# Kernel optimization log

Measured on AMD Instinct MI355X. Metric: run time of the kernel, lower is better.

## Reference

```python
import jax, jax.numpy as jnp
import numpy as np

WS = 8          # window side -> N = 64
DIM = 512
NH = 16
B_ = 1024       # batch * num_windows
CPB_HIDDEN = 512


def _make_coords_table():
    # relative_coords_table: (1, 2*WS-1, 2*WS-1, 2), log-spaced continuous coords
    r = np.arange(-(WS - 1), WS, dtype=np.float32)
    t = np.stack(np.meshgrid(r, r, indexing='ij'), axis=-1)[None]  # (1,15,15,2)
    t = t / (WS - 1)
    t = t * 8.0
    t = np.sign(t) * np.log2(np.abs(t) + 1.0) / np.log2(8.0)
    return t.astype(np.float32)


def _make_rel_pos_index():
    coords = np.stack(np.meshgrid(np.arange(WS), np.arange(WS), indexing='ij'))  # (2,WS,WS)
    cf = coords.reshape(2, -1)                       # (2, N)
    rel = (cf[:, :, None] - cf[:, None, :]).transpose(1, 2, 0).astype(np.int64)  # (N,N,2)
    rel[..., 0] += WS - 1
    rel[..., 1] += WS - 1
    rel[..., 0] *= 2 * WS - 1
    return rel.sum(-1)  # (N, N) int


def setup_inputs() -> dict:
    key = jax.random.key(0)
    ks = jax.random.split(key, 10)
    s_in = 1.0 / np.sqrt(DIM)
    inp = {
        'x': jax.random.normal(ks[0], (B_, WS * WS, DIM), dtype=jnp.float32),
        'qkv_weight': jax.random.normal(ks[1], (3 * DIM, DIM), dtype=jnp.float32) * s_in,
        'q_bias': jnp.zeros((DIM,), dtype=jnp.float32),
        'v_bias': jnp.zeros((DIM,), dtype=jnp.float32),
        'logit_scale': jnp.full((NH, 1, 1), np.log(10.0), dtype=jnp.float32),
        'cpb_w1': jax.random.normal(ks[2], (CPB_HIDDEN, 2), dtype=jnp.float32) * (1.0 / np.sqrt(2.0)),
        'cpb_b1': jnp.zeros((CPB_HIDDEN,), dtype=jnp.float32),
        'cpb_w2': jax.random.normal(ks[3], (NH, CPB_HIDDEN), dtype=jnp.float32) * (1.0 / np.sqrt(CPB_HIDDEN)),
        'proj_w': jax.random.normal(ks[4], (DIM, DIM), dtype=jnp.float32) * s_in,
        'proj_b': jnp.zeros((DIM,), dtype=jnp.float32),
        'rel_coords_table': jnp.asarray(_make_coords_table()),
        'rel_pos_index': jnp.asarray(_make_rel_pos_index()),
    }
    return inp


def reference(x, qkv_weight, q_bias, v_bias, logit_scale, cpb_w1, cpb_b1, cpb_w2,
              proj_w, proj_b, rel_coords_table, rel_pos_index):
    B, N, C = x.shape
    nh = logit_scale.shape[0]
    hd = C // nh

    # qkv projection; bias = [q_bias, 0, v_bias] (k has no bias, Swin-V2 style)
    qkv_bias = jnp.concatenate([q_bias, jnp.zeros_like(q_bias), v_bias])
    qkv = x @ qkv_weight.T + qkv_bias                       # (B, N, 3C)
    qkv = qkv.reshape(B, N, 3, nh, hd).transpose(2, 0, 3, 1, 4)  # (3, B, nh, N, hd)
    q, k, v = qkv[0], qkv[1], qkv[2]

    # continuous position bias MLP: Linear(2,512)+ReLU -> Linear(512,nh, no bias)
    hidden = jax.nn.relu(rel_coords_table @ cpb_w1.T + cpb_b1)  # (1,15,15,512)
    table = (hidden @ cpb_w2.T).reshape(-1, nh)                 # ((2W-1)^2, nh)
    rpb = table[rel_pos_index.reshape(-1)].reshape(N, N, nh).transpose(2, 0, 1)
    rpb = 16.0 * jax.nn.sigmoid(rpb)                            # (nh, N, N)

    # fused attention math: (QK^T)*logit_scale + bias -> softmax -> AV
    scores = jnp.einsum('bhnd,bhmd->bhnm', q, k) * logit_scale.reshape(1, nh, 1, 1)
    scores = scores + rpb[None]
    attn = jax.nn.softmax(scores, axis=-1)
    out = jnp.einsum('bhnm,bhmd->bhnd', attn, v)                # (B, nh, N, hd)
    out = out.transpose(0, 2, 1, 3).reshape(B, N, C)

    return out @ proj_w.T + proj_b
```

## Files before the change

### kernel.cpp

```cpp
#include <hip/hip_runtime.h>
#include <hip/hip_bf16.h>
#include <stdint.h>
#include <stddef.h>


typedef unsigned short ushort_t;
typedef _Float16 half_t;
typedef __attribute__((ext_vector_type(8))) _Float16 half8;
typedef __attribute__((ext_vector_type(4))) float f32x4;

#define MROWS 65536

__device__ __forceinline__ ushort_t h_bits(half_t h) {
  union { half_t h; ushort_t u; } c; c.h = h; return c.u;
}

__device__ __forceinline__ void gload16(const void* g, void* l) {
  __builtin_amdgcn_global_load_lds(
      (const __attribute__((address_space(1))) unsigned int*)g,
      (__attribute__((address_space(3))) unsigned int*)l, 16, 0, 0);
}

__global__ __launch_bounds__(256) void k_split(const float* __restrict__ src,
                                               ushort_t* __restrict__ hi,
                                               ushort_t* __restrict__ lo, int n4) {
  int stride = gridDim.x * blockDim.x;
  for (int i = blockIdx.x * blockDim.x + threadIdx.x; i < n4; i += stride) {
    f32x4 x = reinterpret_cast<const f32x4*>(src)[i];
    ushort_t h4[4], l4[4];
#pragma unroll
    for (int j = 0; j < 4; ++j) {
      half_t hh = (half_t)x[j];
      h4[j] = h_bits(hh);
      l4[j] = h_bits((half_t)(x[j] - (float)hh));
    }
    reinterpret_cast<uint2*>(hi)[i] =
        make_uint2(h4[0] | ((unsigned)h4[1] << 16), h4[2] | ((unsigned)h4[3] << 16));
    reinterpret_cast<uint2*>(lo)[i] =
        make_uint2(l4[0] | ((unsigned)l4[1] << 16), l4[2] | ((unsigned)l4[3] << 16));
  }
}

__global__ __launch_bounds__(256) void k_cpb1(const float* __restrict__ coords,
                                              const float* __restrict__ w1,
                                              const float* __restrict__ b1,
                                              const float* __restrict__ w2,
                                              float* __restrict__ tbl) {
  __shared__ float hid[512];
  int p = blockIdx.x;
  float c0 = coords[2 * p], c1 = coords[2 * p + 1];
  int t = threadIdx.x;
  for (int j = t; j < 512; j += 256) {
    float v = c0 * w1[2 * j] + c1 * w1[2 * j + 1] + b1[j];
    hid[j] = v > 0.f ? v : 0.f;
  }
  __syncthreads();
  int wid = t >> 6, lane = t & 63;
#pragma unroll
  for (int hh = 0; hh < 4; ++hh) {
    int head = wid * 4 + hh;
    float s = 0.f;
    for (int j = lane; j < 512; j += 64) s += hid[j] * w2[head * 512 + j];
#pragma unroll
    for (int off = 32; off > 0; off >>= 1) s += __shfl_xor(s, off);
    if (lane == 0) tbl[p * 16 + head] = 16.f / (1.f + __expf(-s));
  }
}

__global__ __launch_bounds__(256) void k_cpb2(const float* __restrict__ tbl,
                                              const int* __restrict__ ridx,
                                              float* __restrict__ rpb) {
  int idx = blockIdx.x * 256 + threadIdx.x;
  int h = idx >> 12, nm = idx & 4095;
  rpb[idx] = tbl[ridx[nm] * 16 + h];
}

__device__ __forceinline__ int swz(int c, int r) {
  return c ^ (r & 3) ^ ((r >> 2) & 3);
}

__global__ __launch_bounds__(256, 2) void k_qkv(
    const ushort_t* __restrict__ Wh, const ushort_t* __restrict__ Wl,
    const float* __restrict__ X,
    const float* __restrict__ qb, const float* __restrict__ vb,
    ushort_t* __restrict__ oqh, ushort_t* __restrict__ oql,
    ushort_t* __restrict__ okh, ushort_t* __restrict__ okl,
    ushort_t* __restrict__ ovt) {
  __shared__ ushort_t lAh[2][4096];
  __shared__ ushort_t lAl[2][4096];
  __shared__ ushort_t lBh[2][4096];
  __shared__ ushort_t lBl[2][4096];

  int nwg = gridDim.x, bid = blockIdx.x;
  int idx = ((nwg & 7) == 0) ? ((bid & 7) * (nwg >> 3) + (bid >> 3)) : bid;
  int tm = idx % 12, tn = idx / 12;
  int tid = threadIdx.x;
  int wid = tid >> 6, lane = tid & 63;
  int wr = wid >> 1, wc = wid & 1;
  int lr = lane & 15, lq = lane >> 4;

  int rA = tid >> 2, qA = tid & 3;
  size_t gA = (size_t)(tm * 128 + rA) * 512 + (swz(qA, rA) << 3);
  int dA = wid * 512;

  int rB = tid >> 3, qB = tid & 7;
  const float* gB = X + (size_t)(tn * 128 + rB) * 512 + qB * 4;
  int dB = rB * 32 + (swz(qB >> 1, rB) << 3) + ((qB & 1) << 2);

  f32x4 acc[4][4];
#pragma unroll
  for (int i = 0; i < 4; ++i)
#pragma unroll
    for (int j = 0; j < 4; ++j)
#pragma unroll
      for (int r = 0; r < 4; ++r) acc[i][j][r] = 0.f;

  auto stageA = [&](int kk, int bs) {
    gload16(Wh + gA + kk, &lAh[bs][dA]);
    gload16(Wh + gA + 32768 + kk, &lAh[bs][2048 + dA]);
    gload16(Wl + gA + kk, &lAl[bs][dA]);
    gload16(Wl + gA + 32768 + kk, &lAl[bs][2048 + dA]);
  };
  auto loadB = [&](int kk, f32x4* xr) {
#pragma unroll
    for (int s = 0; s < 4; ++s) xr[s] = *(const f32x4*)(gB + s * 16384 + kk);
  };
  auto writeB = [&](const f32x4* xr, int bs) {
#pragma unroll
    for (int s = 0; s < 4; ++s) {
      ushort_t h4[4], l4[4];
#pragma unroll
      for (int e = 0; e < 4; ++e) {
        half_t hh = (half_t)xr[s][e];
        h4[e] = h_bits(hh);
        l4[e] = h_bits((half_t)(xr[s][e] - (float)hh));
      }
      *(uint2*)&lBh[bs][dB + s * 1024] =
          make_uint2(h4[0] | ((unsigned)h4[1] << 16), h4[2] | ((unsigned)h4[3] << 16));
      *(uint2*)&lBl[bs][dB + s * 1024] =
          make_uint2(l4[0] | ((unsigned)l4[1] << 16), l4[2] | ((unsigned)l4[3] << 16));
    }
  };

  f32x4 xr[4];
  stageA(0, 0);
  loadB(0, xr);
  writeB(xr, 0);
  const int c16 = swz(lq, lr) << 3;
#pragma unroll 2
  for (int t = 0; t < 16; ++t) {
    __syncthreads();
    int bs = t & 1;
    if (t < 15) {
      stageA((t + 1) * 32, bs ^ 1);
      loadB((t + 1) * 32, xr);
    }
    half8 ah[4], al[4], bh[4], bl[4];
#pragma unroll
    for (int i = 0; i < 4; ++i) {
      int ro = (wr * 64 + i * 16 + lr) * 32 + c16;
      ah[i] = *(const half8*)&lAh[bs][ro];
      al[i] = *(const half8*)&lAl[bs][ro];
    }
#pragma unroll
    for (int j = 0; j < 4; ++j) {
      int ro = (wc * 64 + j * 16 + lr) * 32 + c16;
      bh[j] = *(const half8*)&lBh[bs][ro];
      bl[j] = *(const half8*)&lBl[bs][ro];
    }
#pragma unroll
    for (int i = 0; i < 4; ++i)
#pragma unroll
      for (int j = 0; j < 4; ++j) {
        acc[i][j] = __builtin_amdgcn_mfma_f32_16x16x32_f16(ah[i], bh[j], acc[i][j], 0, 0, 0);
        acc[i][j] = __builtin_amdgcn_mfma_f32_16x16x32_f16(ah[i], bl[j], acc[i][j], 0, 0, 0);
        acc[i][j] = __builtin_amdgcn_mfma_f32_16x16x32_f16(al[i], bh[j], acc[i][j], 0, 0, 0);
      }
    if (t < 15) writeB(xr, bs ^ 1);
  }

#pragma unroll
  for (int i = 0; i < 4; ++i) {
    int ch0 = tm * 128 + wr * 64 + i * 16 + lq * 4;
#pragma unroll
    for (int j = 0; j < 4; ++j) {
      int tok = tn * 128 + wc * 64 + j * 16 + lr;
      int sec = tm >> 2;
      int h = (ch0 >> 5) & 15, d0 = ch0 & 31;
      int win = tok >> 6, n = tok & 63;
      size_t pr = (size_t)win * 16 + h;
      f32x4 b4;
      if (sec == 0)      b4 = *(const f32x4*)&qb[ch0];
      else if (sec == 2) b4 = *(const f32x4*)&vb[ch0 - 1024];
      else { b4[0] = 0.f; b4[1] = 0.f; b4[2] = 0.f; b4[3] = 0.f; }
      if (sec == 2) {
#pragma unroll
        for (int r = 0; r < 4; ++r) {
          float v = acc[i][j][r] + b4[r];
          ovt[(pr * 32 + d0 + r) * 64 + n] = h_bits((half_t)v);
        }
      } else {
        ushort_t hb[4], lb4[4];
#pragma unroll
        for (int r = 0; r < 4; ++r) {
          float v = acc[i][j][r] + b4[r];
          half_t hh = (half_t)v;
          hb[r] = h_bits(hh);
          lb4[r] = h_bits((half_t)(v - (float)hh));
        }
        uint2 hw = make_uint2(hb[0] | ((unsigned)hb[1] << 16), hb[2] | ((unsigned)hb[3] << 16));
        uint2 lw = make_uint2(lb4[0] | ((unsigned)lb4[1] << 16), lb4[2] | ((unsigned)lb4[3] << 16));
        size_t o = (pr * 64 + n) * 32 + d0;
        if (sec == 0) { *(uint2*)&oqh[o] = hw; *(uint2*)&oql[o] = lw; }
        else          { *(uint2*)&okh[o] = hw; *(uint2*)&okl[o] = lw; }
      }
    }
  }
}

__global__ __launch_bounds__(256, 2) void k_proj(
    const ushort_t* __restrict__ Wh, const ushort_t* __restrict__ Wl,
    const ushort_t* __restrict__ Bp,
    const float* __restrict__ pb, float* __restrict__ outp) {
  __shared__ ushort_t lAh[2][4096];
  __shared__ ushort_t lAl[2][4096];
  __shared__ ushort_t lBh[2][4096];

  int nwg = gridDim.x, bid = blockIdx.x;
  int idx = ((nwg & 7) == 0) ? ((bid & 7) * (nwg >> 3) + (bid >> 3)) : bid;
  int tm = idx % 4, tn = idx / 4;
  int tid = threadIdx.x;
  int wid = tid >> 6, lane = tid & 63;
  int wr = wid >> 1, wc = wid & 1;
  int lr = lane & 15, lq = lane >> 4;

  int rA = tid >> 2, qA = tid & 3;
  int sw = swz(qA, rA) << 3;
  size_t gA = (size_t)(tm * 128 + rA) * 512 + sw;
  size_t gB = (size_t)(tn * 128 + rA) * 512 + sw;
  int dA = wid * 512;

  f32x4 acc[4][4];
#pragma unroll
  for (int i = 0; i < 4; ++i)
#pragma unroll
    for (int j = 0; j < 4; ++j)
#pragma unroll
      for (int r = 0; r < 4; ++r) acc[i][j][r] = 0.f;

  auto stage = [&](int kk, int bs) {
    gload16(Wh + gA + kk, &lAh[bs][dA]);
    gload16(Wh + gA + 32768 + kk, &lAh[bs][2048 + dA]);
    gload16(Wl + gA + kk, &lAl[bs][dA]);
    gload16(Wl + gA + 32768 + kk, &lAl[bs][2048 + dA]);
    gload16(Bp + gB + kk, &lBh[bs][dA]);
    gload16(Bp + gB + 32768 + kk, &lBh[bs][2048 + dA]);
  };

  stage(0, 0);
  const int c16 = swz(lq, lr) << 3;
#pragma unroll 2
  for (int t = 0; t < 16; ++t) {
    __syncthreads();
    int bs = t & 1;
    if (t < 15) stage((t + 1) * 32, bs ^ 1);
    half8 ah[4], al[4], bh[4];
#pragma unroll
    for (int i = 0; i < 4; ++i) {
      int ro = (wr * 64 + i * 16 + lr) * 32 + c16;
      ah[i] = *(const half8*)&lAh[bs][ro];
      al[i] = *(const half8*)&lAl[bs][ro];
    }
#pragma unroll
    for (int j = 0; j < 4; ++j)
      bh[j] = *(const half8*)&lBh[bs][(wc * 64 + j * 16 + lr) * 32 + c16];
#pragma unroll
    for (int i = 0; i < 4; ++i)
#pragma unroll
      for (int j = 0; j < 4; ++j) {
        acc[i][j] = __builtin_amdgcn_mfma_f32_16x16x32_f16(ah[i], bh[j], acc[i][j], 0, 0, 0);
        acc[i][j] = __builtin_amdgcn_mfma_f32_16x16x32_f16(al[i], bh[j], acc[i][j], 0, 0, 0);
      }
  }

#pragma unroll
  for (int i = 0; i < 4; ++i) {
    int ch0 = tm * 128 + wr * 64 + i * 16 + lq * 4;
    f32x4 b4 = *(const f32x4*)&pb[ch0];
#pragma unroll
    for (int j = 0; j < 4; ++j) {
      int tok = tn * 128 + wc * 64 + j * 16 + lr;
      f32x4 o;
#pragma unroll
      for (int r = 0; r < 4; ++r) o[r] = acc[i][j][r] + b4[r];
      *(f32x4*)&outp[(size_t)tok * 512 + ch0] = o;
    }
  }
}

__global__ __launch_bounds__(128) void k_attn(
    const ushort_t* __restrict__ qph, const ushort_t* __restrict__ qpl,
    const ushort_t* __restrict__ kph, const ushort_t* __restrict__ kpl,
    const ushort_t* __restrict__ vt,
    const float* __restrict__ rpb, const float* __restrict__ lsc,
    ushort_t* __restrict__ oh) {
  __shared__ unsigned pw[2][2][64 * 36];
  const int tid = threadIdx.x;
  const int wid = tid >> 6, lane = tid & 63;
  const int pair = blockIdx.x * 2 + wid;
  const int h = pair & 15;
  const int l15 = lane & 15, lq = lane >> 4;
  const size_t base = (size_t)pair * 2048;

  half8 Kh[4], Kl[4], Qh[4], Ql[4];
#pragma unroll
  for (int t4 = 0; t4 < 4; ++t4) {
    int off = (t4 * 16 + l15) * 32 + lq * 8;
    Kh[t4] = *(const half8*)(kph + base + off);
    Kl[t4] = *(const half8*)(kpl + base + off);
    Qh[t4] = *(const half8*)(qph + base + off);
    Ql[t4] = *(const half8*)(qpl + base + off);
  }
  f32x4 st[4][4];
#pragma unroll
  for (int a = 0; a < 4; ++a)
#pragma unroll
    for (int b = 0; b < 4; ++b)
#pragma unroll
      for (int r = 0; r < 4; ++r) st[a][b][r] = 0.f;
#pragma unroll
  for (int kvt = 0; kvt < 4; ++kvt)
#pragma unroll
    for (int qt = 0; qt < 4; ++qt) {
      st[kvt][qt] = __builtin_amdgcn_mfma_f32_16x16x32_f16(Kh[kvt], Qh[qt], st[kvt][qt], 0, 0, 0);
      st[kvt][qt] = __builtin_amdgcn_mfma_f32_16x16x32_f16(Kh[kvt], Ql[qt], st[kvt][qt], 0, 0, 0);
      st[kvt][qt] = __builtin_amdgcn_mfma_f32_16x16x32_f16(Kl[kvt], Qh[qt], st[kvt][qt], 0, 0, 0);
    }

  const float ls = lsc[h];
  const float* rb = rpb + ((size_t)h << 12);
  float mx[4], sm[4], inv[4];
#pragma unroll
  for (int qt = 0; qt < 4; ++qt) {
    int qg = qt * 16 + l15;
    mx[qt] = -1e30f;
#pragma unroll
    for (int kvt = 0; kvt < 4; ++kvt) {
      f32x4 r4 = *(const f32x4*)(rb + qg * 64 + kvt * 16 + lq * 4);
#pragma unroll
      for (int r = 0; r < 4; ++r) {
        float z = st[kvt][qt][r] * ls + r4[r];
        st[kvt][qt][r] = z;
        mx[qt] = fmaxf(mx[qt], z);
      }
    }
    mx[qt] = fmaxf(mx[qt], __shfl_xor(mx[qt], 16));
    mx[qt] = fmaxf(mx[qt], __shfl_xor(mx[qt], 32));
    sm[qt] = 0.f;
#pragma unroll
    for (int kvt = 0; kvt < 4; ++kvt)
#pragma unroll
      for (int r = 0; r < 4; ++r) {
        float e = __expf(st[kvt][qt][r] - mx[qt]);
        st[kvt][qt][r] = e;
        sm[qt] += e;
      }
    sm[qt] += __shfl_xor(sm[qt], 16);
    sm[qt] += __shfl_xor(sm[qt], 32);
    inv[qt] = 1.f / sm[qt];
  }

#pragma unroll
  for (int qt = 0; qt < 4; ++qt) {
    int qg = qt * 16 + l15;
#pragma unroll
    for (int kvt = 0; kvt < 4; ++kvt)
#pragma unroll
      for (int p2 = 0; p2 < 2; ++p2) {
        float pa = st[kvt][qt][2 * p2] * inv[qt];
        float pc = st[kvt][qt][2 * p2 + 1] * inv[qt];
        half_t ha = (half_t)pa, hc = (half_t)pc;
        unsigned wh = h_bits(ha) | ((unsigned)h_bits(hc) << 16);
        unsigned wl = h_bits((half_t)(pa - (float)ha)) |
                      ((unsigned)h_bits((half_t)(pc - (float)hc)) << 16);
        int kv = kvt * 16 + lq * 4 + 2 * p2;
        pw[wid][0][qg * 36 + (kv >> 1)] = wh;
        pw[wid][1][qg * 36 + (kv >> 1)] = wl;
      }
  }

  half8 Vf[2][2];
#pragma unroll
  for (int dt = 0; dt < 2; ++dt)
#pragma unroll
    for (int ks = 0; ks < 2; ++ks)
      Vf[dt][ks] = *(const half8*)(vt + base + (dt * 16 + l15) * 64 + ks * 32 + lq * 8);
  f32x4 ot[2][4];
#pragma unroll
  for (int a = 0; a < 2; ++a)
#pragma unroll
    for (int b = 0; b < 4; ++b)
#pragma unroll
      for (int r = 0; r < 4; ++r) ot[a][b][r] = 0.f;
  const char* pb0 = (const char*)&pw[wid][0][0];
  const char* pb1 = (const char*)&pw[wid][1][0];
#pragma unroll
  for (int qt = 0; qt < 4; ++qt)
#pragma unroll
    for (int ks = 0; ks < 2; ++ks) {
      int off = (qt * 16 + l15) * 144 + ks * 64 + lq * 16;
      half8 Pf = *(const half8*)(pb0 + off);
      half8 Pl = *(const half8*)(pb1 + off);
#pragma unroll
      for (int dt = 0; dt < 2; ++dt) {
        ot[dt][qt] = __builtin_amdgcn_mfma_f32_16x16x32_f16(Vf[dt][ks], Pf, ot[dt][qt], 0, 0, 0);
        ot[dt][qt] = __builtin_amdgcn_mfma_f32_16x16x32_f16(Vf[dt][ks], Pl, ot[dt][qt], 0, 0, 0);
      }
    }

  int win = pair >> 4;
#pragma unroll
  for (int dt = 0; dt < 2; ++dt)
#pragma unroll
    for (int qt = 0; qt < 4; ++qt) {
      int t = win * 64 + qt * 16 + l15;
      int d0 = dt * 16 + lq * 4;
      ushort_t hb[4];
#pragma unroll
      for (int r = 0; r < 4; ++r) hb[r] = h_bits((half_t)ot[dt][qt][r]);
      *(uint2*)&oh[(size_t)t * 512 + h * 32 + d0] =
          make_uint2(hb[0] | ((unsigned)hb[1] << 16), hb[2] | ((unsigned)hb[3] << 16));
    }
}

extern "C" void kernel_launch(void* const* d_in, const int* in_sizes, int n_in,
                              void* d_out, int out_size, void* d_ws, size_t ws_size,
                              hipStream_t stream) {
  const float* x      = (const float*)d_in[0];
  const float* qkvw   = (const float*)d_in[1];
  const float* qb     = (const float*)d_in[2];
  const float* vb     = (const float*)d_in[3];
  const float* lsc    = (const float*)d_in[4];
  const float* w1     = (const float*)d_in[5];
  const float* b1     = (const float*)d_in[6];
  const float* w2     = (const float*)d_in[7];
  const float* pwt    = (const float*)d_in[8];
  const float* pb     = (const float*)d_in[9];
  const float* coords = (const float*)d_in[10];
  const int*   ridx   = (const int*)d_in[11];
  float* out = (float*)d_out;
  char* ws = (char*)d_ws;

  size_t off = 0;
  auto alloc = [&](size_t bytes) {
    size_t r = off;
    off = (off + bytes + 255) & ~(size_t)255;
    return r;
  };
  size_t oWQH = alloc((size_t)1536 * 512 * 2);
  size_t oWQL = alloc((size_t)1536 * 512 * 2);
  size_t oWPH = alloc((size_t)512 * 512 * 2);
  size_t oWPL = alloc((size_t)512 * 512 * 2);
  size_t oRPB = alloc((size_t)16 * 4096 * 4);
  size_t oTBL = alloc((size_t)225 * 16 * 4);
  size_t fixed = off;

  int S = 1;
  while (S <= 32) {
    size_t Ms = (size_t)MROWS / S;
    size_t need = fixed + Ms * 1024 * 6 + 4096;
    if (need <= ws_size) break;
    S <<= 1;
  }
  if (S > 64) S = 64;
  size_t Ms = (size_t)MROWS / S;

  size_t oQH = alloc(Ms * 1024);
  size_t oQL = alloc(Ms * 1024);
  size_t oKH = alloc(Ms * 1024);
  size_t oKL = alloc(Ms * 1024);
  size_t oVT = alloc(Ms * 1024);
  size_t oAO = alloc(Ms * 1024);

  ushort_t* wqh = (ushort_t*)(ws + oWQH);
  ushort_t* wql = (ushort_t*)(ws + oWQL);
  ushort_t* wph = (ushort_t*)(ws + oWPH);
  ushort_t* wpl = (ushort_t*)(ws + oWPL);
  float* rpb = (float*)(ws + oRPB);
  float* tbl = (float*)(ws + oTBL);
  ushort_t* qh = (ushort_t*)(ws + oQH);
  ushort_t* ql = (ushort_t*)(ws + oQL);
  ushort_t* kh = (ushort_t*)(ws + oKH);
  ushort_t* kl = (ushort_t*)(ws + oKL);
  ushort_t* vt = (ushort_t*)(ws + oVT);
  ushort_t* ao = (ushort_t*)(ws + oAO);

  k_split<<<768, 256, 0, stream>>>(qkvw, wqh, wql, 1536 * 512 / 4);
  k_split<<<256, 256, 0, stream>>>(pwt, wph, wpl, 512 * 512 / 4);
  k_cpb1<<<225, 256, 0, stream>>>(coords, w1, b1, w2, tbl);
  k_cpb2<<<256, 256, 0, stream>>>(tbl, ridx, rpb);

  int ntn = (int)(Ms / 128);
  int g0 = 12 * ntn;
  int g1 = 4 * ntn;
  int ga = (int)((Ms / 64) * 16 / 2);

  for (int s = 0; s < S; ++s) {
    const float* xs = x + (size_t)s * Ms * 512;
    k_qkv<<<g0, 256, 0, stream>>>(wqh, wql, xs, qb, vb, qh, ql, kh, kl, vt);
    k_attn<<<ga, 128, 0, stream>>>(qh, ql, kh, kl, vt, rpb, lsc, ao);
    k_proj<<<g1, 256, 0, stream>>>(wph, wpl, ao, pb, out + (size_t)s * Ms * 512);
  }
  (void)in_sizes; (void)n_in; (void)out_size; (void)ws_size;
}
```

Before: 843.8 us.

## Drop low-order split terms from QKV and projection GEMMs, raise occupancy

The QKV GEMM no longer splits the activations into hi/lo halves. It now runs a 32-step loop over the hi and then the lo weight halves against the fp16 activations only, dropping the Wh*Xl correction term. The projection GEMM drops the weight low half entirely and uses only fp16 weights, and a new hi-only split kernel prepares them. LDS per block is halved, launch bounds move to 4 blocks per CU, and MFMA sections are wrapped in s_setprio. Together these cut MFMA work and LDS traffic at the cost of reduced accuracy relative to the fp32 reference.

```diff
diff --git a/kernel.cpp b/kernel.cpp
--- a/kernel.cpp
+++ b/kernel.cpp
@@ -38,6 +38,19 @@
         make_uint2(h4[0] | ((unsigned)h4[1] << 16), h4[2] | ((unsigned)h4[3] << 16));
     reinterpret_cast<uint2*>(lo)[i] =
         make_uint2(l4[0] | ((unsigned)l4[1] << 16), l4[2] | ((unsigned)l4[3] << 16));
+  }
+}
+
+__global__ __launch_bounds__(256) void k_split_h(const float* __restrict__ src,
+                                                 ushort_t* __restrict__ hi, int n4) {
+  int stride = gridDim.x * blockDim.x;
+  for (int i = blockIdx.x * blockDim.x + threadIdx.x; i < n4; i += stride) {
+    f32x4 x = reinterpret_cast<const f32x4*>(src)[i];
+    ushort_t h4[4];
+#pragma unroll
+    for (int j = 0; j < 4; ++j) h4[j] = h_bits((half_t)x[j]);
+    reinterpret_cast<uint2*>(hi)[i] =
+        make_uint2(h4[0] | ((unsigned)h4[1] << 16), h4[2] | ((unsigned)h4[3] << 16));
   }
 }
 
@@ -79,17 +92,15 @@
   return c ^ (r & 3) ^ ((r >> 2) & 3);
 }
 
-__global__ __launch_bounds__(256, 2) void k_qkv(
+__global__ __launch_bounds__(256, 4) void k_qkv(
     const ushort_t* __restrict__ Wh, const ushort_t* __restrict__ Wl,
     const float* __restrict__ X,
     const float* __restrict__ qb, const float* __restrict__ vb,
     ushort_t* __restrict__ oqh, ushort_t* __restrict__ oql,
     ushort_t* __restrict__ okh, ushort_t* __restrict__ okl,
     ushort_t* __restrict__ ovt) {
-  __shared__ ushort_t lAh[2][4096];
-  __shared__ ushort_t lAl[2][4096];
-  __shared__ ushort_t lBh[2][4096];
-  __shared__ ushort_t lBl[2][4096];
+  __shared__ ushort_t lA[2][4096];
+  __shared__ ushort_t lB[2][4096];
 
   int nwg = gridDim.x, bid = blockIdx.x;
   int idx = ((nwg & 7) == 0) ? ((bid & 7) * (nwg >> 3) + (bid >> 3)) : bid;
@@ -115,30 +126,25 @@
 #pragma unroll
       for (int r = 0; r < 4; ++r) acc[i][j][r] = 0.f;
 
-  auto stageA = [&](int kk, int bs) {
-    gload16(Wh + gA + kk, &lAh[bs][dA]);
-    gload16(Wh + gA + 32768 + kk, &lAh[bs][2048 + dA]);
-    gload16(Wl + gA + kk, &lAl[bs][dA]);
-    gload16(Wl + gA + 32768 + kk, &lAl[bs][2048 + dA]);
+  auto stageA = [&](int t2, int bs) {
+    int kk = (t2 & 15) * 32;
+    const ushort_t* W = (t2 >= 16) ? Wl : Wh;
+    gload16(W + gA + kk, &lA[bs][dA]);
+    gload16(W + gA + 32768 + kk, &lA[bs][2048 + dA]);
   };
-  auto loadB = [&](int kk, f32x4* xr) {
+  auto loadB = [&](int t2, f32x4* xr) {
+    int kk = (t2 & 15) * 32;
 #pragma unroll
     for (int s = 0; s < 4; ++s) xr[s] = *(const f32x4*)(gB + s * 16384 + kk);
   };
   auto writeB = [&](const f32x4* xr, int bs) {
 #pragma unroll
     for (int s = 0; s < 4; ++s) {
-      ushort_t h4[4], l4[4];
-#pragma unroll
-      for (int e = 0; e < 4; ++e) {
-        half_t hh = (half_t)xr[s][e];
-        h4[e] = h_bits(hh);
-        l4[e] = h_bits((half_t)(xr[s][e] - (float)hh));
-      }
-      *(uint2*)&lBh[bs][dB + s * 1024] =
+      ushort_t h4[4];
+#pragma unroll
+      for (int e = 0; e < 4; ++e) h4[e] = h_bits((half_t)xr[s][e]);
+      *(uint2*)&lB[bs][dB + s * 1024] =
           make_uint2(h4[0] | ((unsigned)h4[1] << 16), h4[2] | ((unsigned)h4[3] << 16));
-      *(uint2*)&lBl[bs][dB + s * 1024] =
-          make_uint2(l4[0] | ((unsigned)l4[1] << 16), l4[2] | ((unsigned)l4[3] << 16));
     }
   };
 
@@ -148,35 +154,28 @@
   writeB(xr, 0);
   const int c16 = swz(lq, lr) << 3;
 #pragma unroll 2
-  for (int t = 0; t < 16; ++t) {
+  for (int t = 0; t < 32; ++t) {
     __syncthreads();
     int bs = t & 1;
-    if (t < 15) {
-      stageA((t + 1) * 32, bs ^ 1);
-      loadB((t + 1) * 32, xr);
-    }
-    half8 ah[4], al[4], bh[4], bl[4];
-#pragma unroll
-    for (int i = 0; i < 4; ++i) {
-      int ro = (wr * 64 + i * 16 + lr) * 32 + c16;
-      ah[i] = *(const half8*)&lAh[bs][ro];
-      al[i] = *(const half8*)&lAl[bs][ro];
-    }
-#pragma unroll
-    for (int j = 0; j < 4; ++j) {
-      int ro = (wc * 64 + j * 16 + lr) * 32 + c16;
-      bh[j] = *(const half8*)&lBh[bs][ro];
-      bl[j] = *(const half8*)&lBl[bs][ro];
-    }
+    if (t < 31) {
+      stageA(t + 1, bs ^ 1);
+      loadB(t + 1, xr);
+    }
+    half8 af[4], bf[4];
 #pragma unroll
     for (int i = 0; i < 4; ++i)
-#pragma unroll
-      for (int j = 0; j < 4; ++j) {
-        acc[i][j] = __builtin_amdgcn_mfma_f32_16x16x32_f16(ah[i], bh[j], acc[i][j], 0, 0, 0);
-        acc[i][j] = __builtin_amdgcn_mfma_f32_16x16x32_f16(ah[i], bl[j], acc[i][j], 0, 0, 0);
-        acc[i][j] = __builtin_amdgcn_mfma_f32_16x16x32_f16(al[i], bh[j], acc[i][j], 0, 0, 0);
-      }
-    if (t < 15) writeB(xr, bs ^ 1);
+      af[i] = *(const half8*)&lA[bs][(wr * 64 + i * 16 + lr) * 32 + c16];
+#pragma unroll
+    for (int j = 0; j < 4; ++j)
+      bf[j] = *(const half8*)&lB[bs][(wc * 64 + j * 16 + lr) * 32 + c16];
+    __builtin_amdgcn_s_setprio(1);
+#pragma unroll
+    for (int i = 0; i < 4; ++i)
+#pragma unroll
+      for (int j = 0; j < 4; ++j)
+        acc[i][j] = __builtin_amdgcn_mfma_f32_16x16x32_f16(af[i], bf[j], acc[i][j], 0, 0, 0);
+    __builtin_amdgcn_s_setprio(0);
+    if (t < 31) writeB(xr, bs ^ 1);
   }
 
 #pragma unroll
@@ -218,13 +217,12 @@
   }
 }
 
-__global__ __launch_bounds__(256, 2) void k_proj(
-    const ushort_t* __restrict__ Wh, const ushort_t* __restrict__ Wl,
+__global__ __launch_bounds__(256, 4) void k_proj(
+    const ushort_t* __restrict__ Wh,
     const ushort_t* __restrict__ Bp,
     const float* __restrict__ pb, float* __restrict__ outp) {
-  __shared__ ushort_t lAh[2][4096];
-  __shared__ ushort_t lAl[2][4096];
-  __shared__ ushort_t lBh[2][4096];
+  __shared__ ushort_t lA[2][4096];
+  __shared__ ushort_t lB[2][4096];
 
   int nwg = gridDim.x, bid = blockIdx.x;
   int idx = ((nwg & 7) == 0) ? ((bid & 7) * (nwg >> 3) + (bid >> 3)) : bid;
@@ -249,12 +247,10 @@
       for (int r = 0; r < 4; ++r) acc[i][j][r] = 0.f;
 
   auto stage = [&](int kk, int bs) {
-    gload16(Wh + gA + kk, &lAh[bs][dA]);
-    gload16(Wh + gA + 32768 + kk, &lAh[bs][2048 + dA]);
-    gload16(Wl + gA + kk, &lAl[bs][dA]);
-    gload16(Wl + gA + 32768 + kk, &lAl[bs][2048 + dA]);
-    gload16(Bp + gB + kk, &lBh[bs][dA]);
-    gload16(Bp + gB + 32768 + kk, &lBh[bs][2048 + dA]);
+    gload16(Wh + gA + kk, &lA[bs][dA]);
+    gload16(Wh + gA + 32768 + kk, &lA[bs][2048 + dA]);
+    gload16(Bp + gB + kk, &lB[bs][dA]);
+    gload16(Bp + gB + 32768 + kk, &lB[bs][2048 + dA]);
   };
 
   stage(0, 0);
@@ -264,23 +260,20 @@
     __syncthreads();
     int bs = t & 1;
     if (t < 15) stage((t + 1) * 32, bs ^ 1);
-    half8 ah[4], al[4], bh[4];
-#pragma unroll
-    for (int i = 0; i < 4; ++i) {
-      int ro = (wr * 64 + i * 16 + lr) * 32 + c16;
-      ah[i] = *(const half8*)&lAh[bs][ro];
-      al[i] = *(const half8*)&lAl[bs][ro];
-    }
+    half8 af[4], bf[4];
+#pragma unroll
+    for (int i = 0; i < 4; ++i)
+      af[i] = *(const half8*)&lA[bs][(wr * 64 + i * 16 + lr) * 32 + c16];
 #pragma unroll
     for (int j = 0; j < 4; ++j)
-      bh[j] = *(const half8*)&lBh[bs][(wc * 64 + j * 16 + lr) * 32 + c16];
+      bf[j] = *(const half8*)&lB[bs][(wc * 64 + j * 16 + lr) * 32 + c16];
+    __builtin_amdgcn_s_setprio(1);
 #pragma unroll
     for (int i = 0; i < 4; ++i)
 #pragma unroll
-      for (int j = 0; j < 4; ++j) {
-        acc[i][j] = __builtin_amdgcn_mfma_f32_16x16x32_f16(ah[i], bh[j], acc[i][j], 0, 0, 0);
-        acc[i][j] = __builtin_amdgcn_mfma_f32_16x16x32_f16(al[i], bh[j], acc[i][j], 0, 0, 0);
-      }
+      for (int j = 0; j < 4; ++j)
+        acc[i][j] = __builtin_amdgcn_mfma_f32_16x16x32_f16(af[i], bf[j], acc[i][j], 0, 0, 0);
+    __builtin_amdgcn_s_setprio(0);
   }
 
 #pragma unroll
@@ -460,7 +453,6 @@
   size_t oWQH = alloc((size_t)1536 * 512 * 2);
   size_t oWQL = alloc((size_t)1536 * 512 * 2);
   size_t oWPH = alloc((size_t)512 * 512 * 2);
-  size_t oWPL = alloc((size_t)512 * 512 * 2);
   size_t oRPB = alloc((size_t)16 * 4096 * 4);
   size_t oTBL = alloc((size_t)225 * 16 * 4);
   size_t fixed = off;
@@ -485,7 +477,6 @@
   ushort_t* wqh = (ushort_t*)(ws + oWQH);
   ushort_t* wql = (ushort_t*)(ws + oWQL);
   ushort_t* wph = (ushort_t*)(ws + oWPH);
-  ushort_t* wpl = (ushort_t*)(ws + oWPL);
   float* rpb = (float*)(ws + oRPB);
   float* tbl = (float*)(ws + oTBL);
   ushort_t* qh = (ushort_t*)(ws + oQH);
@@ -496,7 +487,7 @@
   ushort_t* ao = (ushort_t*)(ws + oAO);
 
   k_split<<<768, 256, 0, stream>>>(qkvw, wqh, wql, 1536 * 512 / 4);
-  k_split<<<256, 256, 0, stream>>>(pwt, wph, wpl, 512 * 512 / 4);
+  k_split_h<<<256, 256, 0, stream>>>(pwt, wph, 512 * 512 / 4);
   k_cpb1<<<225, 256, 0, stream>>>(coords, w1, b1, w2, tbl);
   k_cpb2<<<256, 256, 0, stream>>>(tbl, ridx, rpb);
 
@@ -509,7 +500,7 @@
     const float* xs = x + (size_t)s * Ms * 512;
     k_qkv<<<g0, 256, 0, stream>>>(wqh, wql, xs, qb, vb, qh, ql, kh, kl, vt);
     k_attn<<<ga, 128, 0, stream>>>(qh, ql, kh, kl, vt, rpb, lsc, ao);
-    k_proj<<<g1, 256, 0, stream>>>(wph, wpl, ao, pb, out + (size_t)s * Ms * 512);
+    k_proj<<<g1, 256, 0, stream>>>(wph, ao, pb, out + (size_t)s * Ms * 512);
   }
   (void)in_sizes; (void)n_in; (void)out_size; (void)ws_size;
 }
```

Result: faster. 728.2 us (-13.7%).
